# Kernel tuning notes

Measured on AMD Instinct MI355X. Metric: run time of the kernel, lower is better.

## Reference

```python
import jax, jax.numpy as jnp
import numpy as np

EMBED = 512
HEADS = 8
FMUL = 4
TAU = 2.0
V_TH = 1.0      # spiking threshold (spikingjelly default)
ALPHA = 2.0     # ATan surrogate alpha (spikingjelly default)
EPS = 1e-5


@jax.custom_vjp
def spike_fn(v):
    # Heaviside spike with ATan surrogate gradient (spikingjelly surrogate.ATan)
    return (v >= V_TH).astype(v.dtype)

def _spike_fwd(v):
    return spike_fn(v), v

def _spike_bwd(v, g):
    t = (jnp.pi / 2.0) * ALPHA * (v - V_TH)
    return (g * (ALPHA / 2.0) / (1.0 + t * t),)

spike_fn.defvjp(_spike_fwd, _spike_bwd)


def layernorm(x, g, b):
    mu = jnp.mean(x, axis=-1, keepdims=True)
    var = jnp.mean(jnp.square(x - mu), axis=-1, keepdims=True)
    return (x - mu) * jax.lax.rsqrt(var + EPS) * g + b


def setup_inputs() -> dict:
    key = jax.random.key(0)
    ks = jax.random.split(key, 12)
    m, s, e = 4, 2048, EMBED
    f = e * FMUL
    sc = 0.02
    return {
        "x":  jax.random.normal(ks[0], (m, s, e), jnp.float32),
        "wq": jax.random.normal(ks[1], (e, e), jnp.float32) * sc,
        "bq": jnp.zeros((e,), jnp.float32),
        "wk": jax.random.normal(ks[2], (e, e), jnp.float32) * sc,
        "bk": jnp.zeros((e,), jnp.float32),
        "wv": jax.random.normal(ks[3], (e, e), jnp.float32) * sc,
        "bv": jnp.zeros((e,), jnp.float32),
        "w1": jax.random.normal(ks[4], (e, f), jnp.float32) * sc,
        "b1": jnp.zeros((f,), jnp.float32),
        "w2": jax.random.normal(ks[5], (f, e), jnp.float32) * sc,
        "b2": jnp.zeros((e,), jnp.float32),
        "g1": jnp.ones((e,), jnp.float32),
        "be1": jnp.zeros((e,), jnp.float32),
        "g2": jnp.ones((e,), jnp.float32),
        "be2": jnp.zeros((e,), jnp.float32),
    }


def reference(x, wq, bq, wk, bk, wv, bv, w1, b1, w2, b2, g1, be1, g2, be2):
    m, s, e = x.shape
    h = HEADS
    d = e // h

    # --- pre-norm attention (NOTE: original has NO 1/sqrt(d) scaling) ---
    n1 = layernorm(x, g1, be1)
    q = (n1 @ wq + bq).reshape(m, s, h, d).transpose(0, 2, 1, 3)  # [m,h,s,d]
    k = (n1 @ wk + bk).reshape(m, s, h, d).transpose(0, 2, 1, 3)
    v = (n1 @ wv + bv).reshape(m, s, h, d).transpose(0, 2, 1, 3)
    scores = jnp.einsum('bhqd,bhkd->bhqk', q, k)       # [m,h,s,s], unscaled
    attn = jax.nn.softmax(scores, axis=-1)
    ctx = jnp.einsum('bhqk,bhkd->bhqd', attn, v)       # [m,h,s,d]
    att_out = ctx.transpose(0, 2, 1, 3).reshape(m, s, e)

    x = x + att_out
    # dropout p=0.4 is identity at inference (eval path in the original)

    # --- FFN with spiking activation ---
    n2 = layernorm(x, g2, be2)
    h1 = n2 @ w1 + b1                                  # [m,s,4e]
    # single-step LIF charge from v=0: v = v + (x - v)/tau = x/tau
    spikes = spike_fn(h1 / TAU)
    return x + (spikes @ w2 + b2)
```

## Files before the change

kernel.cpp:

```cpp
#include <hip/hip_runtime.h>
#include <stdint.h>

#define EMB 512
#define SEQ 2048
#define MB 4
#define NH 8
#define HD 64
#define ROWS (MB*SEQ)
#define MARGIN 0.02f
#define CAP 65536
#define LOG2E 1.44269504f
#define EXPB (-17.3123405f)

typedef unsigned short u16;
typedef __attribute__((ext_vector_type(8))) short bf16x8;
typedef __attribute__((ext_vector_type(4))) float f32x4;
typedef __attribute__((ext_vector_type(2))) unsigned int u32x2;
typedef __attribute__((ext_vector_type(4))) unsigned int u32x4;

union Frag { u32x2 u[2]; bf16x8 v; };
union Frag4 { unsigned u[4]; bf16x8 v; };

__device__ __forceinline__ u16 f2bf(float f) {
  union { float f; unsigned u; } a; a.f = f;
  unsigned r = a.u + 0x7FFFu + ((a.u >> 16) & 1u);
  return (u16)(r >> 16);
}
__device__ __forceinline__ void gld16(const void* g, void* l) {
  __builtin_amdgcn_global_load_lds(
      (const __attribute__((address_space(1))) void*)g,
      (__attribute__((address_space(3))) void*)l, 16, 0, 0);
}


__global__ void k_transpose_all(const float* __restrict__ wq, const float* __restrict__ wk,
                                const float* __restrict__ wv, const float* __restrict__ w1,
                                u16* __restrict__ wqkvT, u16* __restrict__ w1T) {
  __shared__ float tile[32][33];
  int z = blockIdx.z;
  const float* src; u16* dst; int N;
  if (z == 3)      { src = w1; dst = w1T; N = 2048; }
  else if (z == 0) { src = wq; dst = wqkvT;              N = 512; }
  else if (z == 1) { src = wk; dst = wqkvT + 512 * 512;  N = 512; }
  else             { src = wv; dst = wqkvT + 1024 * 512; N = 512; }
  if (blockIdx.x * 32 >= N) return;
  int tx = threadIdx.x, ty = threadIdx.y;
  int k0 = blockIdx.y * 32, n0 = blockIdx.x * 32;
  for (int i = 0; i < 32; i += 8)
    tile[ty + i][tx] = src[(size_t)(k0 + ty + i) * N + n0 + tx];
  __syncthreads();
  for (int i = 0; i < 32; i += 8)
    dst[(size_t)(n0 + ty + i) * 512 + k0 + tx] = f2bf(tile[tx][ty + i]);
}

__global__ __launch_bounds__(256) void k_ln1(const float* __restrict__ x,
    const float* __restrict__ g, const float* __restrict__ b, u16* __restrict__ n1,
    int* __restrict__ cnt) {
  if (blockIdx.x == 0 && threadIdx.x < 2) cnt[threadIdx.x] = 0;
  int wid = threadIdx.x >> 6, lane = threadIdx.x & 63;
  int row = blockIdx.x * 4 + wid;
  const float* xr = x + (size_t)row * EMB + lane * 8;
  f32x4 v0 = *(const f32x4*)xr;
  f32x4 v1 = *(const f32x4*)(xr + 4);
  float s = v0.x+v0.y+v0.z+v0.w + v1.x+v1.y+v1.z+v1.w;
  float q = v0.x*v0.x+v0.y*v0.y+v0.z*v0.z+v0.w*v0.w
          + v1.x*v1.x+v1.y*v1.y+v1.z*v1.z+v1.w*v1.w;
  #pragma unroll
  for (int o = 1; o < 64; o <<= 1) { s += __shfl_xor(s, o); q += __shfl_xor(q, o); }
  float mu = s * (1.0f/512.0f);
  float rs = 1.0f / sqrtf(q * (1.0f/512.0f) - mu*mu + 1e-5f);
  f32x4 ga = *(const f32x4*)(g + lane*8), gb = *(const f32x4*)(g + lane*8 + 4);
  f32x4 ba = *(const f32x4*)(b + lane*8), bb = *(const f32x4*)(b + lane*8 + 4);
  union { u16 h[8]; u32x4 v; } o8;
  o8.h[0] = f2bf((v0.x-mu)*rs*ga.x + ba.x); o8.h[1] = f2bf((v0.y-mu)*rs*ga.y + ba.y);
  o8.h[2] = f2bf((v0.z-mu)*rs*ga.z + ba.z); o8.h[3] = f2bf((v0.w-mu)*rs*ga.w + ba.w);
  o8.h[4] = f2bf((v1.x-mu)*rs*gb.x + bb.x); o8.h[5] = f2bf((v1.y-mu)*rs*gb.y + bb.y);
  o8.h[6] = f2bf((v1.z-mu)*rs*gb.z + bb.z); o8.h[7] = f2bf((v1.w-mu)*rs*gb.w + bb.w);
  *(u32x4*)(n1 + (size_t)row * EMB + lane * 8) = o8.v;
}

__global__ __launch_bounds__(256) void k_ln2(const float* __restrict__ x,
    const float* __restrict__ att, const float* __restrict__ g, const float* __restrict__ b,
    const float* __restrict__ b2, float* __restrict__ x2, u16* __restrict__ n2,
    float* __restrict__ out) {
  int wid = threadIdx.x >> 6, lane = threadIdx.x & 63;
  int row = blockIdx.x * 4 + wid;
  size_t base = (size_t)row * EMB + lane * 8;
  f32x4 v0 = *(const f32x4*)(x + base)     + *(const f32x4*)(att + base);
  f32x4 v1 = *(const f32x4*)(x + base + 4) + *(const f32x4*)(att + base + 4);
  *(f32x4*)(x2 + base) = v0;
  *(f32x4*)(x2 + base + 4) = v1;
  *(f32x4*)(out + base)     = v0 + *(const f32x4*)(b2 + lane*8);
  *(f32x4*)(out + base + 4) = v1 + *(const f32x4*)(b2 + lane*8 + 4);
  float s = v0.x+v0.y+v0.z+v0.w + v1.x+v1.y+v1.z+v1.w;
  float q = v0.x*v0.x+v0.y*v0.y+v0.z*v0.z+v0.w*v0.w
          + v1.x*v1.x+v1.y*v1.y+v1.z*v1.z+v1.w*v1.w;
  #pragma unroll
  for (int o = 1; o < 64; o <<= 1) { s += __shfl_xor(s, o); q += __shfl_xor(q, o); }
  float mu = s * (1.0f/512.0f);
  float rs = 1.0f / sqrtf(q * (1.0f/512.0f) - mu*mu + 1e-5f);
  f32x4 ga = *(const f32x4*)(g + lane*8), gb = *(const f32x4*)(g + lane*8 + 4);
  f32x4 ba = *(const f32x4*)(b + lane*8), bb = *(const f32x4*)(b + lane*8 + 4);
  union { u16 h[8]; u32x4 v; } o8;
  o8.h[0] = f2bf((v0.x-mu)*rs*ga.x + ba.x); o8.h[1] = f2bf((v0.y-mu)*rs*ga.y + ba.y);
  o8.h[2] = f2bf((v0.z-mu)*rs*ga.z + ba.z); o8.h[3] = f2bf((v0.w-mu)*rs*ga.w + ba.w);
  o8.h[4] = f2bf((v1.x-mu)*rs*gb.x + bb.x); o8.h[5] = f2bf((v1.y-mu)*rs*gb.y + bb.y);
  o8.h[6] = f2bf((v1.z-mu)*rs*gb.z + bb.z); o8.h[7] = f2bf((v1.w-mu)*rs*gb.w + bb.w);
  *(u32x4*)(n2 + (size_t)row * EMB + lane * 8) = o8.v;
}

#define GEMM_CORE(A_, Bt_, m0_, n0_)                                           \
  __shared__ u16 As[2][128 * 32];                                              \
  __shared__ u16 Bs[2][128 * 32];                                              \
  int tid = threadIdx.x;                                                       \
  int wid = tid >> 6, lane = tid & 63;                                         \
  int quad = lane >> 4, ln15 = lane & 15;                                      \
  int wm = (wid >> 1) * 64, wn = (wid & 1) * 64;                               \
  int arow = lane >> 2, acol = (lane & 3) * 8;                                 \
  const u16* gA0 = A_  + (size_t)(m0_ + wid * 32 + arow) * 512 + acol;         \
  const u16* gA1 = gA0 + (size_t)16 * 512;                                     \
  const u16* gB0 = Bt_ + (size_t)(n0_ + wid * 32 + arow) * 512 + acol;         \
  const u16* gB1 = gB0 + (size_t)16 * 512;                                     \
  f32x4 acc[4][4] = {};                                                        \
  gld16(gA0, &As[0][(wid * 32) * 32]); gld16(gA1, &As[0][(wid * 32 + 16) * 32]);\
  gld16(gB0, &Bs[0][(wid * 32) * 32]); gld16(gB1, &Bs[0][(wid * 32 + 16) * 32]);\
  for (int kt = 0; kt < 16; kt++) {                                            \
    int cur = kt & 1;                                                          \
    __syncthreads();                                                           \
    if (kt < 15) {                                                             \
      int ko = (kt + 1) * 32;                                                  \
      gld16(gA0 + ko, &As[cur ^ 1][(wid * 32) * 32]);                          \
      gld16(gA1 + ko, &As[cur ^ 1][(wid * 32 + 16) * 32]);                     \
      gld16(gB0 + ko, &Bs[cur ^ 1][(wid * 32) * 32]);                          \
      gld16(gB1 + ko, &Bs[cur ^ 1][(wid * 32 + 16) * 32]);                     \
    }                                                                          \
    bf16x8 af[4], bf[4];                                                       \
    _Pragma("unroll")                                                          \
    for (int i = 0; i < 4; i++) {                                              \
      af[i] = *(const bf16x8*)&As[cur][(wm + i * 16 + ln15) * 32 + quad * 8];  \
      bf[i] = *(const bf16x8*)&Bs[cur][(wn + i * 16 + ln15) * 32 + quad * 8];  \
    }                                                                          \
    _Pragma("unroll")                                                          \
    for (int i = 0; i < 4; i++)                                                \
      _Pragma("unroll")                                                        \
      for (int j = 0; j < 4; j++)                                              \
        acc[i][j] = __builtin_amdgcn_mfma_f32_16x16x32_bf16(af[i], bf[j],      \
                                                            acc[i][j], 0, 0, 0);\
  }                                                                            \
  __syncthreads();

__global__ __launch_bounds__(256) void k_gemm_qkv(
    const u16* __restrict__ A, const u16* __restrict__ Bt,
    const float* __restrict__ bq, const float* __restrict__ bk, const float* __restrict__ bv,
    u16* __restrict__ Qb, u16* __restrict__ Kb, u16* __restrict__ Vtb) {
  int m0 = blockIdx.y * 128, n0 = blockIdx.x * 128;
  GEMM_CORE(A, Bt, m0, n0)
  #pragma unroll
  for (int j = 0; j < 4; j++) {
    int n = n0 + wn + j * 16 + ln15;
    int t = n >> 9, cc = n & 511, head = cc >> 6, dd = cc & 63;
    float bias = (t == 0) ? bq[cc] : ((t == 1) ? bk[cc] : bv[cc]);
    #pragma unroll
    for (int i = 0; i < 4; i++) {
      int row0 = m0 + wm + i * 16 + quad * 4;
      int mm = row0 >> 11, ss0 = row0 & 2047;
      if (t == 2) {
        union { u16 h[4]; u32x2 v; } pk;
        #pragma unroll
        for (int r = 0; r < 4; r++) pk.h[r] = f2bf(acc[i][j][r] + bias);
        *(u32x2*)(Vtb + ((size_t)(mm * 8 + head) * 64 + dd) * 2048 + ss0) = pk.v;
      } else {
        u16* dst = (t == 0) ? Qb : Kb;
        #pragma unroll
        for (int r = 0; r < 4; r++)
          dst[((size_t)(mm * 8 + head) * 2048 + ss0 + r) * 64 + dd] =
              f2bf(acc[i][j][r] + bias);
      }
    }
  }
}

__global__ __launch_bounds__(256) void k_gemm_ffn1(
    const u16* __restrict__ A, const u16* __restrict__ Bt, const float* __restrict__ b1,
    int* __restrict__ cnt, unsigned* __restrict__ spikeL, unsigned* __restrict__ candL) {
  int m0 = blockIdx.y * 128, n0 = blockIdx.x * 128;
  GEMM_CORE(A, Bt, m0, n0)
  #pragma unroll
  for (int j = 0; j < 4; j++) {
    int n = n0 + wn + j * 16 + ln15;
    float bias = b1[n];
    #pragma unroll
    for (int i = 0; i < 4; i++) {
      #pragma unroll
      for (int r = 0; r < 4; r++) {
        int row = m0 + wm + i * 16 + quad * 4 + r;
        float hv = acc[i][j][r] + bias;
        if (hv >= 2.0f - MARGIN) {
          if (hv >= 2.0f + MARGIN) {
            int ix = atomicAdd(&cnt[0], 1);
            if (ix < CAP) spikeL[ix] = (unsigned)(row * 2048 + n);
          } else {
            int ix = atomicAdd(&cnt[1], 1);
            if (ix < CAP) candL[ix] = (unsigned)(row * 2048 + n);
          }
        }
      }
    }
  }
}

#define FLASH_STEP(CUR, KT, DOPRE)                                             \
  do {                                                                         \
    __syncthreads();                                                           \
    if (DOPRE) {                                                               \
      gld16(gK0 + (size_t)((KT) + 1) * 4096, &L.SB[(CUR) ^ 1][0][rb0 * 64]);   \
      gld16(gK1 + (size_t)((KT) + 1) * 4096, &L.SB[(CUR) ^ 1][0][rb1 * 64]);   \
      gld16(gV0 + ((KT) + 1) * 64,           &L.SB[(CUR) ^ 1][1][rb0 * 64]);   \
      gld16(gV1 + ((KT) + 1) * 64,           &L.SB[(CUR) ^ 1][1][rb1 * 64]);   \
    }                                                                          \
    const u16* Kc = L.SB[CUR][0];                                              \
    const u16* Vc = L.SB[CUR][1];                                              \
    f32x4 s4[2][4] = {};                                                       \
    _Pragma("unroll")                                                          \
    for (int t = 0; t < 2; t++)                                                \
      _Pragma("unroll")                                                        \
      for (int j = 0; j < 4; j++) {                                            \
        bf16x8 a = *(const bf16x8*)(Kc + (j * 16 + ln15) * 64 +                \
                                    (((t * 4 + quad) ^ lm) * 8));              \
        s4[0][j] = __builtin_amdgcn_mfma_f32_16x16x32_bf16(a, aQ[0][t].v,      \
                                                           s4[0][j], 0, 0, 0); \
        s4[1][j] = __builtin_amdgcn_mfma_f32_16x16x32_bf16(a, aQ[1][t].v,      \
                                                           s4[1][j], 0, 0, 0); \
      }                                                                        \
    Frag4 bP[2][2];                                                            \
    _Pragma("unroll")                                                          \
    for (int h = 0; h < 2; h++) {                                              \
      unsigned pr[4][4];                                                       \
      _Pragma("unroll")                                                        \
      for (int j = 0; j < 4; j++)                                              \
        _Pragma("unroll")                                                      \
        for (int r = 0; r < 4; r++) {                                          \
          float p = __builtin_amdgcn_exp2f(fmaf(s4[h][j][r], LOG2E, EXPB));    \
          l[h] += p;                                                           \
          union { float f; unsigned u; } cc; cc.f = p;                         \
          pr[j][r] = cc.u + 0x8000u;                                           \
        }                                                                      \
      _Pragma("unroll")                                                        \
      for (int t = 0; t < 2; t++) {                                            \
        bP[h][t].u[0] = __builtin_amdgcn_perm(pr[2*t][1],   pr[2*t][0],   0x07060302u); \
        bP[h][t].u[1] = __builtin_amdgcn_perm(pr[2*t][3],   pr[2*t][2],   0x07060302u); \
        bP[h][t].u[2] = __builtin_amdgcn_perm(pr[2*t+1][1], pr[2*t+1][0], 0x07060302u); \
        bP[h][t].u[3] = __builtin_amdgcn_perm(pr[2*t+1][3], pr[2*t+1][2], 0x07060302u); \
      }                                                                        \
    }                                                                          \
    _Pragma("unroll")                                                          \
    for (int t = 0; t < 2; t++)                                                \
      _Pragma("unroll")                                                        \
      for (int j = 0; j < 4; j++) {                                            \
        int row = j * 16 + ln15;                                               \
        int c0 = 4 * t + (quad >> 1), sub = (quad & 1) * 4;                    \
        Frag aV;                                                               \
        aV.u[0] = *(const u32x2*)(Vc + row * 64 + ((c0 ^ lm) * 8) + sub);      \
        aV.u[1] = *(const u32x2*)(Vc + row * 64 + (((c0 + 2) ^ lm) * 8) + sub);\
        U[0][j] = __builtin_amdgcn_mfma_f32_16x16x32_bf16(aV.v, bP[0][t].v,    \
                                                          U[0][j], 0, 0, 0);   \
        U[1][j] = __builtin_amdgcn_mfma_f32_16x16x32_bf16(aV.v, bP[1][t].v,    \
                                                          U[1][j], 0, 0, 0);   \
      }                                                                        \
  } while (0)

__global__ __launch_bounds__(256, 2) void k_flash(
    const u16* __restrict__ Q, const u16* __restrict__ K,
    const u16* __restrict__ Vt, float* __restrict__ att) {
  __shared__ union {
    u16 SB[2][2][64 * 64];
    float T[4][16 * 68];
  } L;
  int tid = threadIdx.x, wid = tid >> 6, lane = tid & 63;
  int quad = lane >> 4, ln15 = lane & 15, lm = ln15 & 7;
  int qb = blockIdx.x, head = blockIdx.y, mm = blockIdx.z;
  int mh = mm * 8 + head;
  const u16* Qp = Q  + (size_t)mh * SEQ * HD;
  const u16* Kp = K  + (size_t)mh * SEQ * HD;
  const u16* Vp = Vt + (size_t)mh * HD * SEQ;
  int q0 = qb * 128 + wid * 32;

  Frag aQ[2][2];
  #pragma unroll
  for (int h = 0; h < 2; h++)
    #pragma unroll
    for (int t = 0; t < 2; t++) {
      u32x4 g = *(const u32x4*)(Qp + (size_t)(q0 + h * 16 + ln15) * 64 + t * 32 + quad * 8);
      aQ[h][t].u[0].x = g.x; aQ[h][t].u[0].y = g.y;
      aQ[h][t].u[1].x = g.z; aQ[h][t].u[1].y = g.w;
    }

  int srow = lane >> 3;
  int sch  = (lane & 7) ^ (srow & 7);
  int rb0 = wid * 16, rb1 = wid * 16 + 8;
  const u16* gK0 = Kp + (size_t)(rb0 + srow) * 64 + sch * 8;
  const u16* gK1 = Kp + (size_t)(rb1 + srow) * 64 + sch * 8;
  const u16* gV0 = Vp + (size_t)(rb0 + srow) * SEQ + sch * 8;
  const u16* gV1 = Vp + (size_t)(rb1 + srow) * SEQ + sch * 8;

  float l[2] = {0.f, 0.f};
  f32x4 U[2][4] = {};

  gld16(gK0, &L.SB[0][0][rb0 * 64]);
  gld16(gK1, &L.SB[0][0][rb1 * 64]);
  gld16(gV0, &L.SB[0][1][rb0 * 64]);
  gld16(gV1, &L.SB[0][1][rb1 * 64]);

  for (int kt = 0; kt < 32; kt += 2) {
    FLASH_STEP(0, kt, true);
    FLASH_STEP(1, kt + 1, (kt + 1) < 31);
  }
  __syncthreads();

  #pragma unroll
  for (int h = 0; h < 2; h++) {
    float lv = l[h];
    lv += __shfl_xor(lv, 16);
    lv += __shfl_xor(lv, 32);
    float rl = 1.0f / lv;
    float* Tw = L.T[wid];
    #pragma unroll
    for (int j = 0; j < 4; j++)
      *(f32x4*)(Tw + ln15 * 68 + j * 16 + quad * 4) = U[h][j] * rl;
    #pragma unroll
    for (int s = 0; s < 4; s++) {
      f32x4 o = *(const f32x4*)(Tw + (quad * 4 + s) * 68 + ln15 * 4);
      *(f32x4*)(att + ((size_t)mm * SEQ + q0 + h * 16 + quad * 4 + s) * EMB +
                head * 64 + ln15 * 4) = o;
    }
  }
}

__global__ __launch_bounds__(256) void k_fixup(
    const float* __restrict__ x2, const float* __restrict__ w1, const float* __restrict__ b1,
    const float* __restrict__ g2, const float* __restrict__ be2,
    int* __restrict__ cnt, unsigned* __restrict__ spikeL, const unsigned* __restrict__ candL) {
  __shared__ float sb[8];
  int tid = threadIdx.x;
  int nC = cnt[1]; if (nC > CAP) nC = CAP;
  for (int e = blockIdx.x; e < nC; e += gridDim.x) {
    unsigned v = candL[e];
    int row = (int)(v >> 11), col = (int)(v & 2047u);
    const float* xr = x2 + (size_t)row * 512;
    float x0 = xr[tid], x1 = xr[tid + 256];
    float s = x0 + x1, q = x0 * x0 + x1 * x1;
    #pragma unroll
    for (int o = 1; o < 64; o <<= 1) { s += __shfl_xor(s, o); q += __shfl_xor(q, o); }
    if ((tid & 63) == 0) { sb[tid >> 6] = s; sb[4 + (tid >> 6)] = q; }
    __syncthreads();
    float st = sb[0] + sb[1] + sb[2] + sb[3];
    float qt = sb[4] + sb[5] + sb[6] + sb[7];
    __syncthreads();
    float mu = st * (1.f / 512.f);
    float rs = 1.f / sqrtf(qt * (1.f / 512.f) - mu * mu + 1e-5f);
    float na = (x0 - mu) * rs * g2[tid] + be2[tid];
    float nb = (x1 - mu) * rs * g2[tid + 256] + be2[tid + 256];
    float dd = na * w1[(size_t)tid * 2048 + col] + nb * w1[(size_t)(tid + 256) * 2048 + col];
    #pragma unroll
    for (int o = 1; o < 64; o <<= 1) dd += __shfl_xor(dd, o);
    if ((tid & 63) == 0) sb[tid >> 6] = dd;
    __syncthreads();
    if (tid == 0) {
      float hv = sb[0] + sb[1] + sb[2] + sb[3] + b1[col];
      if (hv >= 2.0f) { int ix = atomicAdd(&cnt[0], 1); if (ix < CAP) spikeL[ix] = v; }
    }
    __syncthreads();
  }
}

__global__ void k_apply(const float* __restrict__ w2, const int* __restrict__ cnt,
                        const unsigned* __restrict__ spikeL, float* __restrict__ out) {
  int n = cnt[0]; if (n > CAP) n = CAP;
  int tid = threadIdx.x;
  for (int e = blockIdx.x; e < n; e += gridDim.x) {
    unsigned v = spikeL[e];
    int row = (int)(v >> 11), col = (int)(v & 2047u);
    atomicAdd(&out[(size_t)row * 512 + tid * 2 + 0], w2[(size_t)col * 512 + tid * 2 + 0]);
    atomicAdd(&out[(size_t)row * 512 + tid * 2 + 1], w2[(size_t)col * 512 + tid * 2 + 1]);
  }
}


extern "C" void kernel_launch(void* const* d_in, const int* in_sizes, int n_in,
                              void* d_out, int out_size, void* d_ws, size_t ws_size,
                              hipStream_t stream) {
  (void)in_sizes; (void)n_in; (void)out_size; (void)ws_size;
  const float* x   = (const float*)d_in[0];
  const float* wq  = (const float*)d_in[1];
  const float* bq  = (const float*)d_in[2];
  const float* wk  = (const float*)d_in[3];
  const float* bk  = (const float*)d_in[4];
  const float* wv  = (const float*)d_in[5];
  const float* bv  = (const float*)d_in[6];
  const float* w1  = (const float*)d_in[7];
  const float* b1  = (const float*)d_in[8];
  const float* w2  = (const float*)d_in[9];
  const float* b2  = (const float*)d_in[10];
  const float* g1  = (const float*)d_in[11];
  const float* be1 = (const float*)d_in[12];
  const float* g2  = (const float*)d_in[13];
  const float* be2 = (const float*)d_in[14];
  float* out = (float*)d_out;

  char* w = (char*)d_ws;
  size_t off = 0;
  auto take = [&](size_t bytes) { char* p = w + off; off += (bytes + 255) & ~(size_t)255; return p; };
  int*      cnt    = (int*)take(256);
  u16*      n1     = (u16*)take((size_t)ROWS * EMB * 2);
  u16*      wqkvT  = (u16*)take((size_t)1536 * 512 * 2);
  u16*      w1T    = (u16*)take((size_t)2048 * 512 * 2);
  u16*      Qb     = (u16*)take((size_t)MB * NH * SEQ * HD * 2);
  u16*      Kb     = (u16*)take((size_t)MB * NH * SEQ * HD * 2);
  u16*      Vtb    = (u16*)take((size_t)MB * NH * SEQ * HD * 2);
  float*    att    = (float*)take((size_t)ROWS * EMB * 4);
  float*    x2     = (float*)take((size_t)ROWS * EMB * 4);
  u16*      n2     = (u16*)take((size_t)ROWS * EMB * 2);
  unsigned* spikeL = (unsigned*)take((size_t)CAP * 4);
  unsigned* candL  = (unsigned*)take((size_t)CAP * 4);

  k_transpose_all<<<dim3(64, 16, 4), dim3(32, 8), 0, stream>>>(wq, wk, wv, w1, wqkvT, w1T);
  k_ln1<<<ROWS / 4, 256, 0, stream>>>(x, g1, be1, n1, cnt);
  k_gemm_qkv<<<dim3(12, 64), 256, 0, stream>>>(n1, wqkvT, bq, bk, bv, Qb, Kb, Vtb);
  k_flash<<<dim3(16, 8, 4), 256, 0, stream>>>(Qb, Kb, Vtb, att);
  k_ln2<<<ROWS / 4, 256, 0, stream>>>(x, att, g2, be2, b2, x2, n2, out);
  k_gemm_ffn1<<<dim3(16, 64), 256, 0, stream>>>(n2, w1T, b1, cnt, spikeL, candL);
  k_fixup<<<256, 256, 0, stream>>>(x2, w1, b1, g2, be2, cnt, spikeL, candL);
  k_apply<<<128, 256, 0, stream>>>(w2, cnt, spikeL, out);
}
```

Before: 213.3 us.

## Stage two key tiles per barrier in flash kernel and compact transpose grid

The flash attention loop now loads two 64-key K/V tiles per double-buffered stage, which halves the number of block-wide barriers. It also seeds the first MFMA with a zero accumulator and drops the round-to-nearest bias when packing P to bf16, so P is now truncated. The weight-transpose launch becomes a 1D grid of 1792 blocks instead of a 3D grid where many blocks exited early. LDS use per block doubles to 64KB, which may limit occupancy, and the truncation slightly changes numerics.

```diff
diff --git a/kernel.cpp b/kernel.cpp
--- a/kernel.cpp
+++ b/kernel.cpp
@@ -37,15 +37,18 @@
                                 const float* __restrict__ wv, const float* __restrict__ w1,
                                 u16* __restrict__ wqkvT, u16* __restrict__ w1T) {
   __shared__ float tile[32][33];
-  int z = blockIdx.z;
-  const float* src; u16* dst; int N;
-  if (z == 3)      { src = w1; dst = w1T; N = 2048; }
-  else if (z == 0) { src = wq; dst = wqkvT;              N = 512; }
-  else if (z == 1) { src = wk; dst = wqkvT + 512 * 512;  N = 512; }
-  else             { src = wv; dst = wqkvT + 1024 * 512; N = 512; }
-  if (blockIdx.x * 32 >= N) return;
+  int b = blockIdx.x;
+  const float* src; u16* dst; int N, bx, by;
+  if (b < 768) {
+    int z = b >> 8, rem = b & 255; bx = rem & 15; by = rem >> 4; N = 512;
+    src = (z == 0) ? wq : ((z == 1) ? wk : wv);
+    dst = wqkvT + z * 512 * 512;
+  } else {
+    int rem = b - 768; bx = rem & 63; by = rem >> 6; N = 2048;
+    src = w1; dst = w1T;
+  }
   int tx = threadIdx.x, ty = threadIdx.y;
-  int k0 = blockIdx.y * 32, n0 = blockIdx.x * 32;
+  int k0 = by * 32, n0 = bx * 32;
   for (int i = 0; i < 32; i += 8)
     tile[ty + i][tx] = src[(size_t)(k0 + ty + i) * N + n0 + tx];
   __syncthreads();
@@ -209,29 +212,35 @@
   }
 }
 
-#define FLASH_STEP(CUR, KT, DOPRE)                                             \
+#define F_STAGE(BUF, T0)                                                       \
   do {                                                                         \
-    __syncthreads();                                                           \
-    if (DOPRE) {                                                               \
-      gld16(gK0 + (size_t)((KT) + 1) * 4096, &L.SB[(CUR) ^ 1][0][rb0 * 64]);   \
-      gld16(gK1 + (size_t)((KT) + 1) * 4096, &L.SB[(CUR) ^ 1][0][rb1 * 64]);   \
-      gld16(gV0 + ((KT) + 1) * 64,           &L.SB[(CUR) ^ 1][1][rb0 * 64]);   \
-      gld16(gV1 + ((KT) + 1) * 64,           &L.SB[(CUR) ^ 1][1][rb1 * 64]);   \
+    gld16(gK0 + (size_t)(T0)       * 4096, &L.SB[BUF][0][0][rb0 * 64]);        \
+    gld16(gK1 + (size_t)(T0)       * 4096, &L.SB[BUF][0][0][rb1 * 64]);        \
+    gld16(gK0 + (size_t)((T0) + 1) * 4096, &L.SB[BUF][0][1][rb0 * 64]);        \
+    gld16(gK1 + (size_t)((T0) + 1) * 4096, &L.SB[BUF][0][1][rb1 * 64]);        \
+    gld16(gV0 + (T0) * 64,       &L.SB[BUF][1][0][rb0 * 64]);                  \
+    gld16(gV1 + (T0) * 64,       &L.SB[BUF][1][0][rb1 * 64]);                  \
+    gld16(gV0 + ((T0) + 1) * 64, &L.SB[BUF][1][1][rb0 * 64]);                  \
+    gld16(gV1 + ((T0) + 1) * 64, &L.SB[BUF][1][1][rb1 * 64]);                  \
+  } while (0)
+
+#define F_INNER(BUF, SUB)                                                      \
+  do {                                                                         \
+    const u16* Kc = L.SB[BUF][0][SUB];                                         \
+    const u16* Vc = L.SB[BUF][1][SUB];                                         \
+    f32x4 s4[2][4];                                                            \
+    _Pragma("unroll")                                                          \
+    for (int j = 0; j < 4; j++) {                                              \
+      bf16x8 a = *(const bf16x8*)(Kc + (j * 16 + ln15) * 64 + ((quad ^ lm) * 8)); \
+      s4[0][j] = __builtin_amdgcn_mfma_f32_16x16x32_bf16(a, aQ[0][0].v, z4, 0, 0, 0); \
+      s4[1][j] = __builtin_amdgcn_mfma_f32_16x16x32_bf16(a, aQ[1][0].v, z4, 0, 0, 0); \
     }                                                                          \
-    const u16* Kc = L.SB[CUR][0];                                              \
-    const u16* Vc = L.SB[CUR][1];                                              \
-    f32x4 s4[2][4] = {};                                                       \
-    _Pragma("unroll")                                                          \
-    for (int t = 0; t < 2; t++)                                                \
-      _Pragma("unroll")                                                        \
-      for (int j = 0; j < 4; j++) {                                            \
-        bf16x8 a = *(const bf16x8*)(Kc + (j * 16 + ln15) * 64 +                \
-                                    (((t * 4 + quad) ^ lm) * 8));              \
-        s4[0][j] = __builtin_amdgcn_mfma_f32_16x16x32_bf16(a, aQ[0][t].v,      \
-                                                           s4[0][j], 0, 0, 0); \
-        s4[1][j] = __builtin_amdgcn_mfma_f32_16x16x32_bf16(a, aQ[1][t].v,      \
-                                                           s4[1][j], 0, 0, 0); \
-      }                                                                        \
+    _Pragma("unroll")                                                          \
+    for (int j = 0; j < 4; j++) {                                              \
+      bf16x8 a = *(const bf16x8*)(Kc + (j * 16 + ln15) * 64 + (((4 + quad) ^ lm) * 8)); \
+      s4[0][j] = __builtin_amdgcn_mfma_f32_16x16x32_bf16(a, aQ[0][1].v, s4[0][j], 0, 0, 0); \
+      s4[1][j] = __builtin_amdgcn_mfma_f32_16x16x32_bf16(a, aQ[1][1].v, s4[1][j], 0, 0, 0); \
+    }                                                                          \
     Frag4 bP[2][2];                                                            \
     _Pragma("unroll")                                                          \
     for (int h = 0; h < 2; h++) {                                              \
@@ -243,7 +252,7 @@
           float p = __builtin_amdgcn_exp2f(fmaf(s4[h][j][r], LOG2E, EXPB));    \
           l[h] += p;                                                           \
           union { float f; unsigned u; } cc; cc.f = p;                         \
-          pr[j][r] = cc.u + 0x8000u;                                           \
+          pr[j][r] = cc.u;                                                     \
         }                                                                      \
       _Pragma("unroll")                                                        \
       for (int t = 0; t < 2; t++) {                                            \
@@ -269,11 +278,19 @@
       }                                                                        \
   } while (0)
 
+#define F_STEP(CUR, S)                                                         \
+  do {                                                                         \
+    __syncthreads();                                                           \
+    if ((S) < 15) F_STAGE((CUR) ^ 1, 2 * (S) + 2);                             \
+    F_INNER(CUR, 0);                                                           \
+    F_INNER(CUR, 1);                                                           \
+  } while (0)
+
 __global__ __launch_bounds__(256, 2) void k_flash(
     const u16* __restrict__ Q, const u16* __restrict__ K,
     const u16* __restrict__ Vt, float* __restrict__ att) {
   __shared__ union {
-    u16 SB[2][2][64 * 64];
+    u16 SB[2][2][2][64 * 64];
     float T[4][16 * 68];
   } L;
   int tid = threadIdx.x, wid = tid >> 6, lane = tid & 63;
@@ -294,6 +311,7 @@
       aQ[h][t].u[0].x = g.x; aQ[h][t].u[0].y = g.y;
       aQ[h][t].u[1].x = g.z; aQ[h][t].u[1].y = g.w;
     }
+  const f32x4 z4 = {0.f, 0.f, 0.f, 0.f};
 
   int srow = lane >> 3;
   int sch  = (lane & 7) ^ (srow & 7);
@@ -306,14 +324,10 @@
   float l[2] = {0.f, 0.f};
   f32x4 U[2][4] = {};
 
-  gld16(gK0, &L.SB[0][0][rb0 * 64]);
-  gld16(gK1, &L.SB[0][0][rb1 * 64]);
-  gld16(gV0, &L.SB[0][1][rb0 * 64]);
-  gld16(gV1, &L.SB[0][1][rb1 * 64]);
-
-  for (int kt = 0; kt < 32; kt += 2) {
-    FLASH_STEP(0, kt, true);
-    FLASH_STEP(1, kt + 1, (kt + 1) < 31);
+  F_STAGE(0, 0);
+  for (int it = 0; it < 8; it++) {
+    F_STEP(0, 2 * it);
+    F_STEP(1, 2 * it + 1);
   }
   __syncthreads();
 
@@ -423,7 +437,7 @@
   unsigned* spikeL = (unsigned*)take((size_t)CAP * 4);
   unsigned* candL  = (unsigned*)take((size_t)CAP * 4);
 
-  k_transpose_all<<<dim3(64, 16, 4), dim3(32, 8), 0, stream>>>(wq, wk, wv, w1, wqkvT, w1T);
+  k_transpose_all<<<1792, dim3(32, 8), 0, stream>>>(wq, wk, wv, w1, wqkvT, w1T);
   k_ln1<<<ROWS / 4, 256, 0, stream>>>(x, g1, be1, n1, cnt);
   k_gemm_qkv<<<dim3(12, 64), 256, 0, stream>>>(n1, wqkvT, bq, bk, bv, Qb, Kb, Vtb);
   k_flash<<<dim3(16, 8, 4), 256, 0, stream>>>(Qb, Kb, Vtb, att);
```

New measurement: 211.2 us. No clear change (-1.0%).
